# Kernel tuning notes

Hardware: AMD Instinct MI355X
Metric: run time of the kernel (lower is better)

## Reference

```python
import jax, jax.numpy as jnp
import numpy as np

B, H, S, DK = 2, 8, 4096, 64


def setup_inputs() -> dict:
    key = jax.random.key(0)
    kq, kk, kv = jax.random.split(key, 3)
    Q = jax.random.normal(kq, (B, H, S, DK), dtype=jnp.float32)
    K = jax.random.normal(kk, (B, H, S, DK), dtype=jnp.float32)
    V = jax.random.normal(kv, (B, H, S, DK), dtype=jnp.float32)
    attn_mask = jnp.zeros((1,), dtype=bool)  # accepted but unused by the module
    return {"Q": Q, "K": K, "V": V, "attn_mask": attn_mask}


def reference(Q, K, V, attn_mask):
    d_k = Q.shape[-1]
    scale = 1.0 / np.sqrt(d_k).astype(np.float32)
    # scores: [b, h, q, k] -- full O(n^2) matrix, as in the original
    scores = jnp.einsum('bhqd,bhkd->bhqk', Q, K) * scale
    attn = jax.nn.softmax(scores, axis=-1)
    context = jnp.einsum('bhqk,bhkd->bhqd', attn, V)
    return (context, attn)
```

## Files before the change

kernel.cpp:

```cpp
#include <hip/hip_runtime.h>
#include <hip/hip_bf16.h>


typedef __bf16 bf16x8 __attribute__((ext_vector_type(8)));
typedef __bf16 bf16x4 __attribute__((ext_vector_type(4)));
typedef float f32x4 __attribute__((ext_vector_type(4)));

#define BH 16
#define SEQ 4096
#define DKD 64
#define LOG2E 1.44269504088896f

__global__ void cvt_bf16_kernel(const float* __restrict__ src,
                                __bf16* __restrict__ dst, int n4, float scale) {
    int i = blockIdx.x * blockDim.x + threadIdx.x;
    if (i < n4) {
        const float4 v = reinterpret_cast<const float4*>(src)[i];
        bf16x4 o;
        o[0] = (__bf16)(v.x * scale); o[1] = (__bf16)(v.y * scale);
        o[2] = (__bf16)(v.z * scale); o[3] = (__bf16)(v.w * scale);
        reinterpret_cast<bf16x4*>(dst)[i] = o;
    }
}

__global__ void transpose_v_kernel(const float* __restrict__ V,
                                   __bf16* __restrict__ Vt) {
    __shared__ __bf16 T[DKD][72];
    const int head = blockIdx.y;
    const int s0 = blockIdx.x * 64;
    const int t = threadIdx.x;
    const float* vp = V + ((size_t)head * SEQ + s0) * DKD;
#pragma unroll
    for (int i = 0; i < 16; ++i) {
        int j = i * 256 + t;
        T[j & 63][j >> 6] = (__bf16)vp[j];
    }
    __syncthreads();
    __bf16* op = Vt + (size_t)head * DKD * SEQ + s0;
#pragma unroll
    for (int i = 0; i < 16; ++i) {
        int j = i * 256 + t;
        op[(size_t)(j >> 6) * SEQ + (j & 63)] = T[j >> 6][j & 63];
    }
}

__global__ __launch_bounds__(256, 4) void attn_kernel(
    const __bf16* __restrict__ Qb, const __bf16* __restrict__ Kb,
    const __bf16* __restrict__ Vt, float* __restrict__ out_ctx,
    float* __restrict__ out_attn) {
    __shared__ __align__(16) float Pf[2][2][16][68];
    __shared__ float Lsum[4][16];

    const int tid = threadIdx.x;
    const int w = tid >> 6;
    const int lane = tid & 63;
    const int c16 = lane & 15;
    const int g = lane >> 4;
    const int qsub = w & 1;
    const int khalf = w >> 1;

    const int wg = blockIdx.x;
    const int head = ((wg & 7) << 1) | ((wg >> 3) & 1);
    const int qblk = wg >> 4;
    const int qbase = qblk * 32 + qsub * 16;

    const __bf16* qp = Qb + ((size_t)head * SEQ + qbase + c16) * DKD + g * 8;
    const bf16x8 qf0 = *reinterpret_cast<const bf16x8*>(qp);
    const bf16x8 qf1 = *reinterpret_cast<const bf16x8*>(qp + 32);

    const __bf16* kbase = Kb + (size_t)head * SEQ * DKD;
    const __bf16* vbase = Vt + (size_t)head * DKD * SEQ;
    float* attn_p = out_attn + ((size_t)head * SEQ + qbase) * SEQ;

    float lsum = 0.f;
    for (int t = 0; t < 32; ++t) {
        const int kt = (khalf * 32 + t) * 64;
#pragma unroll
        for (int ct = 0; ct < 4; ++ct) {
            const __bf16* kp = kbase + (size_t)(kt + ct * 16 + c16) * DKD + g * 8;
            bf16x8 kf0 = *reinterpret_cast<const bf16x8*>(kp);
            bf16x8 kf1 = *reinterpret_cast<const bf16x8*>(kp + 32);
            f32x4 a = (f32x4){0.f, 0.f, 0.f, 0.f};
            a = __builtin_amdgcn_mfma_f32_16x16x32_bf16(kf0, qf0, a, 0, 0, 0);
            a = __builtin_amdgcn_mfma_f32_16x16x32_bf16(kf1, qf1, a, 0, 0, 0);
            float e0 = __builtin_amdgcn_exp2f(a[0] * LOG2E);
            float e1 = __builtin_amdgcn_exp2f(a[1] * LOG2E);
            float e2 = __builtin_amdgcn_exp2f(a[2] * LOG2E);
            float e3 = __builtin_amdgcn_exp2f(a[3] * LOG2E);
            lsum += (e0 + e1) + (e2 + e3);
        }
    }
    lsum += __shfl_xor(lsum, 16);
    lsum += __shfl_xor(lsum, 32);
    if (g == 0) Lsum[w][c16] = lsum;
    __syncthreads();

    if (w < 2) {
        const float inv_l = __builtin_amdgcn_rcpf(Lsum[w][c16] + Lsum[w ^ 2][c16]);

        f32x4 o[4];
#pragma unroll
        for (int dt = 0; dt < 4; ++dt) o[dt] = (f32x4){0.f, 0.f, 0.f, 0.f};

        auto computeS = [&](int t, float(*Pbuf)[68]) {
            const int kt = t * 64;
#pragma unroll
            for (int h = 0; h < 2; ++h) {
                f32x4 acc[2];
#pragma unroll
                for (int ct = 0; ct < 2; ++ct) {
                    acc[ct] = (f32x4){0.f, 0.f, 0.f, 0.f};
                    const __bf16* kp =
                        kbase + (size_t)(kt + h * 32 + ct * 16 + c16) * DKD + g * 8;
                    bf16x8 kf0 = *reinterpret_cast<const bf16x8*>(kp);
                    bf16x8 kf1 = *reinterpret_cast<const bf16x8*>(kp + 32);
                    acc[ct] = __builtin_amdgcn_mfma_f32_16x16x32_bf16(kf0, qf0, acc[ct], 0, 0, 0);
                    acc[ct] = __builtin_amdgcn_mfma_f32_16x16x32_bf16(kf1, qf1, acc[ct], 0, 0, 0);
                }
#pragma unroll
                for (int ct = 0; ct < 2; ++ct) {
                    f32x4 p;
#pragma unroll
                    for (int r = 0; r < 4; ++r)
                        p[r] = __builtin_amdgcn_exp2f(acc[ct][r] * LOG2E) * inv_l;
                    *reinterpret_cast<f32x4*>(&Pbuf[c16][h * 32 + ct * 16 + g * 4]) = p;
                }
            }
        };

        auto pvTile = [&](int t, const float(*Pbuf)[68]) {
            const int kt = t * 64;
            f32x4 a0 = *reinterpret_cast<const f32x4*>(&Pbuf[c16][g * 8]);
            f32x4 a1 = *reinterpret_cast<const f32x4*>(&Pbuf[c16][g * 8 + 4]);
            f32x4 b0 = *reinterpret_cast<const f32x4*>(&Pbuf[c16][g * 8 + 32]);
            f32x4 b1 = *reinterpret_cast<const f32x4*>(&Pbuf[c16][g * 8 + 36]);
            bf16x8 pb0, pb1;
#pragma unroll
            for (int j = 0; j < 4; ++j) {
                pb0[j] = (__bf16)a0[j]; pb0[j + 4] = (__bf16)a1[j];
                pb1[j] = (__bf16)b0[j]; pb1[j + 4] = (__bf16)b1[j];
            }
#pragma unroll
            for (int dt = 0; dt < 4; ++dt) {
                const __bf16* vp = vbase + (size_t)(dt * 16 + c16) * SEQ + kt + g * 8;
                bf16x8 vf0 = *reinterpret_cast<const bf16x8*>(vp);
                bf16x8 vf1 = *reinterpret_cast<const bf16x8*>(vp + 32);
                o[dt] = __builtin_amdgcn_mfma_f32_16x16x32_bf16(vf0, pb0, o[dt], 0, 0, 0);
                o[dt] = __builtin_amdgcn_mfma_f32_16x16x32_bf16(vf1, pb1, o[dt], 0, 0, 0);
            }
        };

        computeS(0, Pf[0][w]);
        asm volatile("s_waitcnt lgkmcnt(0)" ::: "memory");
        __builtin_amdgcn_s_barrier();
        for (int t = 1; t < 64; ++t) {
            computeS(t, Pf[t & 1][w]);
            pvTile(t - 1, Pf[(t - 1) & 1][w]);
            asm volatile("s_waitcnt lgkmcnt(0)" ::: "memory");
            __builtin_amdgcn_s_barrier();
        }
        pvTile(63, Pf[1][w]);

        float* ctx_p = out_ctx + ((size_t)head * SEQ + qbase) * DKD;
#pragma unroll
        for (int dt = 0; dt < 4; ++dt)
            *reinterpret_cast<f32x4*>(ctx_p + (size_t)c16 * DKD + dt * 16 + g * 4) = o[dt];
    } else {
        const int srow = lane >> 2;
        const int scN = (lane & 3) * 4;
        const float* srcbase = &Pf[0][w & 1][0][0];
        const float* srcalt = &Pf[1][w & 1][0][0];
        for (int t = 0; t < 64; ++t) {
            __builtin_amdgcn_s_barrier();
            __builtin_amdgcn_sched_barrier(0);
            const float* src = (t & 1) ? srcalt : srcbase;
            const int kt = t * 64;
#pragma unroll
            for (int j = 0; j < 4; ++j) {
                f32x4 v = *reinterpret_cast<const f32x4*>(src + srow * 68 + j * 16 + scN);
                *reinterpret_cast<f32x4*>(attn_p + (size_t)srow * SEQ + kt + j * 16 + scN) = v;
            }
        }
    }
}

extern "C" void kernel_launch(void* const* d_in, const int* in_sizes, int n_in,
                              void* d_out, int out_size, void* d_ws, size_t ws_size,
                              hipStream_t stream) {
    const float* Q = (const float*)d_in[0];
    const float* K = (const float*)d_in[1];
    const float* V = (const float*)d_in[2];
    float* out = (float*)d_out;

    const size_t nElem = (size_t)BH * SEQ * DKD;
    __bf16* Qb = (__bf16*)d_ws;
    __bf16* Kb = Qb + nElem;
    __bf16* Vt = Kb + nElem;

    float* out_ctx = out;
    float* out_attn = out + nElem;

    const int n4 = (int)(nElem / 4);
    cvt_bf16_kernel<<<dim3((n4 + 255) / 256), dim3(256), 0, stream>>>(Q, Qb, n4, 0.125f);
    cvt_bf16_kernel<<<dim3((n4 + 255) / 256), dim3(256), 0, stream>>>(K, Kb, n4, 1.0f);
    transpose_v_kernel<<<dim3(64, BH), dim3(256), 0, stream>>>(V, Vt);
    attn_kernel<<<dim3(BH * SEQ / 32), dim3(256), 0, stream>>>(Qb, Kb, Vt, out_ctx, out_attn);
}
```

Baseline: 775.9 us.

## Stage P as bf16 in LDS and batch four key tiles per barrier

Probabilities are now stored in shared memory as bf16 rather than fp32, and each barrier covers a group of four 64-key tiles instead of one. This cuts the number of barriers from 64 to 16 and removes the separate conversion step before the PV MFMA. The writer waves now emit whole 1 KB rows per instruction, which gives wider, more contiguous global stores. In exchange, the attention output is rounded to bf16 precision before being written as fp32, which reduces accuracy, and the PV pipelining inside each group is shallower.

```diff
diff --git a/kernel.cpp b/kernel.cpp
--- a/kernel.cpp
+++ b/kernel.cpp
@@ -9,6 +9,7 @@
 #define BH 16
 #define SEQ 4096
 #define DKD 64
+#define GSTRIDE 264
 #define LOG2E 1.44269504088896f
 
 __global__ void cvt_bf16_kernel(const float* __restrict__ src,
@@ -48,7 +49,7 @@
     const __bf16* __restrict__ Qb, const __bf16* __restrict__ Kb,
     const __bf16* __restrict__ Vt, float* __restrict__ out_ctx,
     float* __restrict__ out_attn) {
-    __shared__ __align__(16) float Pf[2][2][16][68];
+    __shared__ __align__(16) __bf16 Pg[2][2][16][GSTRIDE];
     __shared__ float Lsum[4][16];
 
     const int tid = threadIdx.x;
@@ -102,7 +103,7 @@
 #pragma unroll
         for (int dt = 0; dt < 4; ++dt) o[dt] = (f32x4){0.f, 0.f, 0.f, 0.f};
 
-        auto computeS = [&](int t, float(*Pbuf)[68]) {
+        auto computeS = [&](int t, int s, __bf16(*Pbuf)[GSTRIDE]) {
             const int kt = t * 64;
 #pragma unroll
             for (int h = 0; h < 2; ++h) {
@@ -119,27 +120,20 @@
                 }
 #pragma unroll
                 for (int ct = 0; ct < 2; ++ct) {
-                    f32x4 p;
+                    bf16x4 pb;
 #pragma unroll
                     for (int r = 0; r < 4; ++r)
-                        p[r] = __builtin_amdgcn_exp2f(acc[ct][r] * LOG2E) * inv_l;
-                    *reinterpret_cast<f32x4*>(&Pbuf[c16][h * 32 + ct * 16 + g * 4]) = p;
+                        pb[r] = (__bf16)(__builtin_amdgcn_exp2f(acc[ct][r] * LOG2E) * inv_l);
+                    *reinterpret_cast<bf16x4*>(
+                        &Pbuf[c16][s * 64 + h * 32 + ct * 16 + g * 4]) = pb;
                 }
             }
         };
 
-        auto pvTile = [&](int t, const float(*Pbuf)[68]) {
+        auto pvTile = [&](int t, int s, const __bf16(*Pbuf)[GSTRIDE]) {
             const int kt = t * 64;
-            f32x4 a0 = *reinterpret_cast<const f32x4*>(&Pbuf[c16][g * 8]);
-            f32x4 a1 = *reinterpret_cast<const f32x4*>(&Pbuf[c16][g * 8 + 4]);
-            f32x4 b0 = *reinterpret_cast<const f32x4*>(&Pbuf[c16][g * 8 + 32]);
-            f32x4 b1 = *reinterpret_cast<const f32x4*>(&Pbuf[c16][g * 8 + 36]);
-            bf16x8 pb0, pb1;
-#pragma unroll
-            for (int j = 0; j < 4; ++j) {
-                pb0[j] = (__bf16)a0[j]; pb0[j + 4] = (__bf16)a1[j];
-                pb1[j] = (__bf16)b0[j]; pb1[j + 4] = (__bf16)b1[j];
-            }
+            bf16x8 pb0 = *reinterpret_cast<const bf16x8*>(&Pbuf[c16][s * 64 + g * 8]);
+            bf16x8 pb1 = *reinterpret_cast<const bf16x8*>(&Pbuf[c16][s * 64 + g * 8 + 32]);
 #pragma unroll
             for (int dt = 0; dt < 4; ++dt) {
                 const __bf16* vp = vbase + (size_t)(dt * 16 + c16) * SEQ + kt + g * 8;
@@ -150,35 +144,39 @@
             }
         };
 
-        computeS(0, Pf[0][w]);
-        asm volatile("s_waitcnt lgkmcnt(0)" ::: "memory");
-        __builtin_amdgcn_s_barrier();
-        for (int t = 1; t < 64; ++t) {
-            computeS(t, Pf[t & 1][w]);
-            pvTile(t - 1, Pf[(t - 1) & 1][w]);
+        for (int grp = 0; grp < 16; ++grp) {
+            __bf16(*buf)[GSTRIDE] = Pg[grp & 1][w];
+            const int t0 = grp * 4;
+            computeS(t0 + 0, 0, buf);
+            computeS(t0 + 1, 1, buf);
+            pvTile(t0 + 0, 0, buf);
+            computeS(t0 + 2, 2, buf);
+            pvTile(t0 + 1, 1, buf);
+            computeS(t0 + 3, 3, buf);
+            pvTile(t0 + 2, 2, buf);
+            pvTile(t0 + 3, 3, buf);
             asm volatile("s_waitcnt lgkmcnt(0)" ::: "memory");
             __builtin_amdgcn_s_barrier();
+            __builtin_amdgcn_sched_barrier(0);
         }
-        pvTile(63, Pf[1][w]);
 
         float* ctx_p = out_ctx + ((size_t)head * SEQ + qbase) * DKD;
 #pragma unroll
         for (int dt = 0; dt < 4; ++dt)
             *reinterpret_cast<f32x4*>(ctx_p + (size_t)c16 * DKD + dt * 16 + g * 4) = o[dt];
     } else {
-        const int srow = lane >> 2;
-        const int scN = (lane & 3) * 4;
-        const float* srcbase = &Pf[0][w & 1][0][0];
-        const float* srcalt = &Pf[1][w & 1][0][0];
-        for (int t = 0; t < 64; ++t) {
+        for (int grp = 0; grp < 16; ++grp) {
             __builtin_amdgcn_s_barrier();
             __builtin_amdgcn_sched_barrier(0);
-            const float* src = (t & 1) ? srcalt : srcbase;
-            const int kt = t * 64;
-#pragma unroll
-            for (int j = 0; j < 4; ++j) {
-                f32x4 v = *reinterpret_cast<const f32x4*>(src + srow * 68 + j * 16 + scN);
-                *reinterpret_cast<f32x4*>(attn_p + (size_t)srow * SEQ + kt + j * 16 + scN) = v;
+            const __bf16(*buf)[GSTRIDE] = Pg[grp & 1][qsub];
+            const int k0 = grp * 256;
+#pragma unroll
+            for (int r = 0; r < 16; ++r) {
+                bf16x4 pb = *reinterpret_cast<const bf16x4*>(&buf[r][lane * 4]);
+                f32x4 v;
+#pragma unroll
+                for (int j = 0; j < 4; ++j) v[j] = (float)pb[j];
+                *reinterpret_cast<f32x4*>(attn_p + (size_t)r * SEQ + k0 + lane * 4) = v;
             }
         }
     }
```

Measured after the change: 876.6 us. +13.0%, slower.
